# Performance work log

Measured on AMD Instinct MI355X. Metric: run time of the kernel, lower is better.

## Reference

```python
import jax, jax.numpy as jnp
import numpy as np

D_MODEL = 1024
NHEAD = 16
DK = D_MODEL // NHEAD
B, LQ, LK = 4, 2048, 2048


def setup_inputs() -> dict:
    key = jax.random.key(0)
    ks = jax.random.split(key, 11)
    s = 1.0 / np.sqrt(D_MODEL)
    inp = {
        "q": jax.random.normal(ks[0], (B, LQ, D_MODEL), jnp.float32),
        "k": jax.random.normal(ks[1], (B, LK, D_MODEL), jnp.float32),
        "v": jax.random.normal(ks[2], (B, LK, D_MODEL), jnp.float32),
        "attn_mask": jnp.triu(jnp.ones((LQ, LK), dtype=bool), k=1),  # True = masked (causal)
        "Wq": jax.random.normal(ks[3], (D_MODEL, D_MODEL), jnp.float32) * s,
        "bq": jnp.zeros((D_MODEL,), jnp.float32),
        "Wk": jax.random.normal(ks[4], (D_MODEL, D_MODEL), jnp.float32) * s,
        "bk": jnp.zeros((D_MODEL,), jnp.float32),
        "Wv": jax.random.normal(ks[5], (D_MODEL, D_MODEL), jnp.float32) * s,
        "bv": jnp.zeros((D_MODEL,), jnp.float32),
        "Wo": jax.random.normal(ks[6], (D_MODEL, D_MODEL), jnp.float32) * s,
        "bo": jnp.zeros((D_MODEL,), jnp.float32),
    }
    return inp


def _split_heads(x, L):
    # (B, L, D) -> (B, H, L, dk)
    return x.reshape(B, L, NHEAD, DK).transpose(0, 2, 1, 3)


def reference(q, k, v, attn_mask, Wq, bq, Wk, bk, Wv, bv, Wo, bo):
    qh = _split_heads(q @ Wq + bq, LQ)
    kh = _split_heads(k @ Wk + bk, LK)
    vh = _split_heads(v @ Wv + bv, LK)
    scale = 1.0 / np.sqrt(DK).astype(np.float32)
    scores = jnp.einsum("bhqd,bhkd->bhqk", qh, kh) * scale
    scores = jnp.where(attn_mask[None, None, :, :], -jnp.inf, scores)
    attn = jax.nn.softmax(scores, axis=-1)
    ctx = jnp.einsum("bhqk,bhkd->bhqd", attn, vh)
    ctx = ctx.transpose(0, 2, 1, 3).reshape(B, LQ, D_MODEL)
    return ctx @ Wo + bo
```

## Files before the change

### kernel.cpp

```cpp
#include <hip/hip_runtime.h>

#define D_MODEL 1024
#define NHEAD 16
#define DKH 64
#define BATCH 4
#define SEQ 2048
#define MROWS (BATCH*SEQ)

typedef unsigned short u16;
typedef __attribute__((ext_vector_type(8))) short bf16x8;
typedef __attribute__((ext_vector_type(4))) float f32x4;

__device__ __forceinline__ u16 f2bf(float f) {
  union { float f; unsigned int u; } x; x.f = f;
  unsigned int r = x.u + 0x7FFFu + ((x.u >> 16) & 1u);
  return (u16)(r >> 16);
}
__device__ __forceinline__ u16 f2bf_fast(float f) {
  union { float f; unsigned int u; } x; x.f = f;
  return (u16)((x.u + 0x7FFFu) >> 16);
}

__device__ __forceinline__ f32x4 mfma16(bf16x8 a, bf16x8 b, f32x4 c) {
  return __builtin_amdgcn_mfma_f32_16x16x32_bf16(a, b, c, 0, 0, 0);
}

__device__ __forceinline__ void gld_lds16(const void* g, void* l) {
  __builtin_amdgcn_global_load_lds((const __attribute__((address_space(1))) unsigned int*)g,
                                   (__attribute__((address_space(3))) unsigned int*)l, 16, 0, 0);
}

__global__ __launch_bounds__(256) void prep_kernel(
    const float* __restrict__ q, const float* __restrict__ k, const float* __restrict__ v,
    const float* __restrict__ W0, const float* __restrict__ W1,
    const float* __restrict__ W2, const float* __restrict__ W3,
    u16* __restrict__ oq, u16* __restrict__ ok, u16* __restrict__ ov,
    u16* __restrict__ T0, u16* __restrict__ T1,
    u16* __restrict__ T2, u16* __restrict__ T3) {
  const int blk = blockIdx.x;
  const int tid = threadIdx.x;
  if (blk < 24576) {
    const int seg = blk >> 13;
    const int bi = blk & 8191;
    const float* in = (seg == 0) ? q : (seg == 1) ? k : v;
    u16* out = (seg == 0) ? oq : (seg == 1) ? ok : ov;
    int i = (bi * 256 + tid) * 4;
    float4 vv = *(const float4*)(in + i);
    ushort4 o;
    o.x = f2bf(vv.x); o.y = f2bf(vv.y); o.z = f2bf(vv.z); o.w = f2bf(vv.w);
    *(ushort4*)(out + i) = o;
  } else {
    __shared__ float tile[32][33];
    const int t = blk - 24576;
    const int z = t >> 10;
    const int rem = t & 1023;
    const float* W = (z == 0) ? W0 : (z == 1) ? W1 : (z == 2) ? W2 : W3;
    u16* Wt = (z == 0) ? T0 : (z == 1) ? T1 : (z == 2) ? T2 : T3;
    const int bx = (rem & 31) * 32, by = (rem >> 5) * 32;
    const int tx = tid & 31, ty = tid >> 5;
#pragma unroll
    for (int j = 0; j < 32; j += 8)
      tile[ty + j][tx] = W[(size_t)(by + ty + j) * D_MODEL + bx + tx];
    __syncthreads();
#pragma unroll
    for (int j = 0; j < 32; j += 8)
      Wt[(size_t)(bx + ty + j) * D_MODEL + by + tx] = f2bf(tile[tx][ty + j]);
  }
}

template <typename Epi>
__device__ __forceinline__ void gemm_pipe(const u16* __restrict__ Ap,
                                          const u16* __restrict__ Bp,
                                          int m0, int n0g, Epi epi) {
  __shared__ u16 As[2][128 * 64];
  __shared__ u16 Bs[2][128 * 64];
  const int tid = threadIdx.x;
  const int lane = tid & 63;
  const int w = tid >> 6;
  const int wm = w >> 1, wn = w & 1;
  const int lo = lane & 15, g = lane >> 4;
  const int swz = (lo & 7) << 4;
  const int sg = (tid & 7) ^ ((tid >> 3) & 7);
  const int srow = tid >> 3;

  f32x4 acc[4][4] = {};

  auto STAGE_A = [&](int buf, int tt, int j) {
    int row = j * 32 + srow;
    gld_lds16(Ap + (size_t)(m0 + row) * D_MODEL + tt * 64 + sg * 8,
              &As[buf][j * 2048 + tid * 8]);
  };
  auto STAGE_B = [&](int buf, int tt, int j) {
    int row = j * 32 + srow;
    gld_lds16(Bp + (size_t)(n0g + row) * D_MODEL + tt * 64 + sg * 8,
              &Bs[buf][j * 2048 + tid * 8]);
  };

  STAGE_A(0, 0, 0); STAGE_A(0, 0, 1); STAGE_A(0, 0, 2); STAGE_A(0, 0, 3);
  STAGE_B(0, 0, 0); STAGE_B(0, 0, 1); STAGE_B(0, 0, 2); STAGE_B(0, 0, 3);
  STAGE_B(1, 1, 0); STAGE_B(1, 1, 1); STAGE_B(1, 1, 2); STAGE_B(1, 1, 3);
  asm volatile("s_waitcnt vmcnt(4)" ::: "memory");
  __builtin_amdgcn_s_barrier();

  int cur = 0;
#pragma unroll 1
  for (int t = 0; t < 16; ++t) {
    const int nb = cur ^ 1;
    const char* ab = (const char*)&As[cur][0];
    const char* bb2 = (const char*)&Bs[cur][0];

    bf16x8 bf[4][2], af[2][2];
#pragma unroll
    for (int n = 0; n < 4; ++n) {
      int row = wn * 64 + n * 16 + lo;
      bf[n][0] = *(const bf16x8*)(bb2 + row * 128 + ((g * 16) ^ swz));
      bf[n][1] = *(const bf16x8*)(bb2 + row * 128 + ((64 + g * 16) ^ swz));
    }
#pragma unroll
    for (int m = 0; m < 2; ++m) {
      int row = wm * 64 + m * 16 + lo;
      af[m][0] = *(const bf16x8*)(ab + row * 128 + ((g * 16) ^ swz));
      af[m][1] = *(const bf16x8*)(ab + row * 128 + ((64 + g * 16) ^ swz));
    }
    if (t + 1 < 16) {
      STAGE_A(nb, t + 1, 0); STAGE_A(nb, t + 1, 1);
      STAGE_A(nb, t + 1, 2); STAGE_A(nb, t + 1, 3);
    }
    __builtin_amdgcn_s_barrier();
    __builtin_amdgcn_s_setprio(1);
#pragma unroll
    for (int s2 = 0; s2 < 2; ++s2)
#pragma unroll
      for (int m = 0; m < 2; ++m)
#pragma unroll
        for (int n = 0; n < 4; ++n)
          acc[m][n] = mfma16(af[m][s2], bf[n][s2], acc[m][n]);
    __builtin_amdgcn_s_setprio(0);
    __builtin_amdgcn_s_barrier();

    bf16x8 af2[2][2];
#pragma unroll
    for (int m = 0; m < 2; ++m) {
      int row = wm * 64 + (m + 2) * 16 + lo;
      af2[m][0] = *(const bf16x8*)(ab + row * 128 + ((g * 16) ^ swz));
      af2[m][1] = *(const bf16x8*)(ab + row * 128 + ((64 + g * 16) ^ swz));
    }
    if (t + 2 < 16) {
      STAGE_B(cur, t + 2, 0); STAGE_B(cur, t + 2, 1);
      STAGE_B(cur, t + 2, 2); STAGE_B(cur, t + 2, 3);
    }
    __builtin_amdgcn_s_barrier();
    __builtin_amdgcn_s_setprio(1);
#pragma unroll
    for (int s2 = 0; s2 < 2; ++s2)
#pragma unroll
      for (int m = 0; m < 2; ++m)
#pragma unroll
        for (int n = 0; n < 4; ++n)
          acc[m + 2][n] = mfma16(af2[m][s2], bf[n][s2], acc[m + 2][n]);
    __builtin_amdgcn_s_setprio(0);
    if (t + 2 < 16) asm volatile("s_waitcnt vmcnt(4)" ::: "memory");
    else            asm volatile("s_waitcnt vmcnt(0)" ::: "memory");
    __builtin_amdgcn_s_barrier();
    cur = nb;
  }

  epi(acc, wm, wn, lo, g);
}

__global__ __launch_bounds__(256, 2) void gemm_qkv_kernel(
    const u16* __restrict__ Aq, const u16* __restrict__ Ak, const u16* __restrict__ Av,
    const u16* __restrict__ Wt,
    const float* __restrict__ bq, const float* __restrict__ bk, const float* __restrict__ bv,
    u16* __restrict__ Qhd, u16* __restrict__ Khd, u16* __restrict__ Vhd, float qscale) {
  const int flat = blockIdx.x;
  const int swzb = (flat & 7) * 192 + (flat >> 3);
  const int m0 = (swzb / 24) * 128;
  const int n0g = (swzb % 24) * 128;
  const int chunk = n0g >> 10;
  const u16* Ap = (chunk == 0) ? Aq : (chunk == 1) ? Ak : Av;
  const float* bias = (chunk == 0) ? bq : (chunk == 1) ? bk : bv;
  const float scale = (chunk == 0) ? qscale : 1.0f;

  gemm_pipe(Ap, Wt, m0, n0g,
    [&](f32x4 (&acc)[4][4], int wm, int wn, int lo, int g) {
#pragma unroll
      for (int m = 0; m < 4; ++m)
#pragma unroll
        for (int n = 0; n < 4; ++n) {
          int row0 = m0 + wm * 64 + m * 16 + g * 4;
          int colc = (n0g & 1023) + wn * 64 + n * 16 + lo;
          int hh = colc >> 6, d = colc & 63;
          int bb = row0 >> 11;
          float v0 = (acc[m][n][0] + bias[colc]) * scale;
          float v1 = (acc[m][n][1] + bias[colc]) * scale;
          float v2 = (acc[m][n][2] + bias[colc]) * scale;
          float v3 = (acc[m][n][3] + bias[colc]) * scale;
          if (chunk < 2) {
            u16* out = chunk ? Khd : Qhd;
#pragma unroll
            for (int i = 0; i < 4; ++i) {
              int l = (row0 + i) & 2047;
              float vi = (i == 0) ? v0 : (i == 1) ? v1 : (i == 2) ? v2 : v3;
              out[(((size_t)(bb * NHEAD + hh)) * SEQ + l) * DKH + d] = f2bf(vi);
            }
          } else {
            int l = row0 & 2047;
            int kh = (l >> 2) & 7;
            int pos = (l & ~31) | ((2 * (kh & 3) + (kh >> 2)) << 2);
            ushort4 o;
            o.x = f2bf(v0); o.y = f2bf(v1); o.z = f2bf(v2); o.w = f2bf(v3);
            *(ushort4*)&Vhd[(((size_t)(bb * NHEAD + hh)) * DKH + d) * SEQ + pos] = o;
          }
        }
    });
}

__global__ __launch_bounds__(256, 2) void gemm_o_kernel(
    const u16* __restrict__ A, const u16* __restrict__ Bt,
    const float* __restrict__ bias, float* __restrict__ Cout) {
  const int flat = blockIdx.x;
  const int swzb = (flat & 7) * 64 + (flat >> 3);
  const int m0 = (swzb >> 3) * 128;
  const int n0g = (swzb & 7) * 128;

  gemm_pipe(A, Bt, m0, n0g,
    [&](f32x4 (&acc)[4][4], int wm, int wn, int lo, int g) {
#pragma unroll
      for (int m = 0; m < 4; ++m)
#pragma unroll
        for (int n = 0; n < 4; ++n) {
          int row0 = m0 + wm * 64 + m * 16 + g * 4;
          int col = n0g + wn * 64 + n * 16 + lo;
          float bcol = bias[col];
#pragma unroll
          for (int i = 0; i < 4; ++i)
            Cout[(size_t)(row0 + i) * D_MODEL + col] = acc[m][n][i] + bcol;
        }
    });
}

__global__ __launch_bounds__(256, 3) void attn_kernel(
    const u16* __restrict__ Qh, const u16* __restrict__ Kh,
    const u16* __restrict__ Vt, u16* __restrict__ ctx) {
  const int blk = blockIdx.x;
  const int xcd = blk & 7;
  const int local = blk >> 3;
  const int qb = 15 - (local >> 3);
  const int head = xcd * 8 + (local & 7);
  const int b = head >> 4, h = head & (NHEAD - 1);

  const int tid = threadIdx.x;
  const int lane = tid & 63;
  const int w = tid >> 6;
  const int lo = lane & 15, g = lane >> 4;
  const int swz = (lo & 7) << 4;

  __shared__ u16 Ks[3][64 * 64];
  __shared__ u16 Vs[3][64 * 64];

  const size_t hoff = ((size_t)(b * NHEAD + h)) * SEQ * DKH;
  const u16* Qp = Qh + hoff;
  const u16* Kp = Kh + hoff;
  const u16* Vp = Vt + hoff;

  const int nt = 2 * qb + 2;
  const int qmin = qb * 128 + w * 32;

  bf16x8 aq[2][2];
#pragma unroll
  for (int qs = 0; qs < 2; ++qs)
#pragma unroll
    for (int cc = 0; cc < 2; ++cc)
      aq[qs][cc] = *(const bf16x8*)(Qp + (size_t)(qmin + qs * 16 + lo) * DKH + cc * 32 + g * 8);

  const int r_lo = lane >> 3;
  const int sgr = (lane & 7) ^ r_lo;

  auto STAGE = [&](int buf, int t64) {
#pragma unroll
    for (int j = 0; j < 2; ++j) {
      int row = w * 16 + j * 8 + r_lo;
      gld_lds16(Kp + (size_t)(t64 * 64 + row) * DKH + sgr * 8, &Ks[buf][(w * 2 + j) * 512]);
      gld_lds16(Vp + (size_t)row * SEQ + t64 * 64 + sgr * 8, &Vs[buf][(w * 2 + j) * 512]);
    }
  };

  STAGE(0, 0);
  STAGE(1, 1);
  asm volatile("s_waitcnt vmcnt(0)" ::: "memory");
  __builtin_amdgcn_s_barrier();

  f32x4 c[2][4] = {};
  float m_run[2] = {-1e30f, -1e30f}, l_run[2] = {0.f, 0.f};
  int cur = 0;

  for (int kt = 0; kt < nt; ++kt) {
    int b2 = cur + 2; if (b2 >= 3) b2 -= 3;
    if (kt + 2 < nt) STAGE(b2, kt + 2);

    f32x4 s[2][4] = {};
#pragma unroll
    for (int kn = 0; kn < 4; ++kn) {
      const char* krow = (const char*)&Ks[cur][(kn * 16 + lo) * 64];
#pragma unroll
      for (int cc = 0; cc < 2; ++cc) {
        bf16x8 ak = *(const bf16x8*)(krow + ((cc * 64 + g * 16) ^ swz));
        s[0][kn] = mfma16(ak, aq[0][cc], s[0][kn]);
        s[1][kn] = mfma16(ak, aq[1][cc], s[1][kn]);
      }
    }

    if (kt >= nt - 2) {
#pragma unroll
      for (int qs = 0; qs < 2; ++qs) {
        int q = qmin + qs * 16 + lo;
#pragma unroll
        for (int kn = 0; kn < 4; ++kn)
#pragma unroll
          for (int i = 0; i < 4; ++i) {
            int key = kt * 64 + kn * 16 + g * 4 + i;
            if (key > q) s[qs][kn][i] = -1e30f;
          }
      }
    }

    bf16x8 pb[2][2];
#pragma unroll
    for (int qs = 0; qs < 2; ++qs) {
      float mx = s[qs][0][0];
#pragma unroll
      for (int kn = 0; kn < 4; ++kn)
#pragma unroll
        for (int i = 0; i < 4; ++i) mx = fmaxf(mx, s[qs][kn][i]);
      mx = fmaxf(mx, __shfl_xor(mx, 16));
      mx = fmaxf(mx, __shfl_xor(mx, 32));
      if (!__all(mx - m_run[qs] <= 8.0f)) {
        float mnew = fmaxf(m_run[qs], mx);
        float al = __builtin_amdgcn_exp2f(m_run[qs] - mnew);
        m_run[qs] = mnew;
        l_run[qs] *= al;
#pragma unroll
        for (int dn = 0; dn < 4; ++dn) {
          c[qs][dn][0] *= al; c[qs][dn][1] *= al;
          c[qs][dn][2] *= al; c[qs][dn][3] *= al;
        }
      }
      const float mq = m_run[qs];
      float rs = 0.f;
#pragma unroll
      for (int kn = 0; kn < 4; ++kn)
#pragma unroll
        for (int i = 0; i < 4; ++i) {
          float p = __builtin_amdgcn_exp2f(s[qs][kn][i] - mq);
          s[qs][kn][i] = p;
          rs += p;
        }
      rs += __shfl_xor(rs, 16);
      rs += __shfl_xor(rs, 32);
      l_run[qs] += rs;
#pragma unroll
      for (int kc = 0; kc < 2; ++kc) {
        bf16x8 t;
        t[0] = (short)f2bf_fast(s[qs][2 * kc][0]);
        t[1] = (short)f2bf_fast(s[qs][2 * kc][1]);
        t[2] = (short)f2bf_fast(s[qs][2 * kc][2]);
        t[3] = (short)f2bf_fast(s[qs][2 * kc][3]);
        t[4] = (short)f2bf_fast(s[qs][2 * kc + 1][0]);
        t[5] = (short)f2bf_fast(s[qs][2 * kc + 1][1]);
        t[6] = (short)f2bf_fast(s[qs][2 * kc + 1][2]);
        t[7] = (short)f2bf_fast(s[qs][2 * kc + 1][3]);
        pb[qs][kc] = t;
      }
    }

#pragma unroll
    for (int kc = 0; kc < 2; ++kc)
#pragma unroll
      for (int dn = 0; dn < 4; ++dn) {
        const char* vrow = (const char*)&Vs[cur][(dn * 16 + lo) * 64];
        bf16x8 av = *(const bf16x8*)(vrow + ((kc * 64 + g * 16) ^ swz));
        c[0][dn] = mfma16(av, pb[0][kc], c[0][dn]);
        c[1][dn] = mfma16(av, pb[1][kc], c[1][dn]);
      }

    if (kt + 1 < nt) {
      if (kt + 2 < nt) asm volatile("s_waitcnt vmcnt(4)" ::: "memory");
      else             asm volatile("s_waitcnt vmcnt(0)" ::: "memory");
      __builtin_amdgcn_s_barrier();
    }
    cur = (cur == 2) ? 0 : cur + 1;
  }

#pragma unroll
  for (int qs = 0; qs < 2; ++qs) {
    const float rl = 1.0f / l_run[qs];
    const int q = qmin + qs * 16 + lo;
#pragma unroll
    for (int dn = 0; dn < 4; ++dn) {
      ushort4 o;
      o.x = f2bf(c[qs][dn][0] * rl);
      o.y = f2bf(c[qs][dn][1] * rl);
      o.z = f2bf(c[qs][dn][2] * rl);
      o.w = f2bf(c[qs][dn][3] * rl);
      *(ushort4*)&ctx[((size_t)(b * SEQ + q)) * D_MODEL + h * DKH + dn * 16 + g * 4] = o;
    }
  }
}

extern "C" void kernel_launch(void* const* d_in, const int* in_sizes, int n_in,
                              void* d_out, int out_size, void* d_ws, size_t ws_size,
                              hipStream_t stream) {
  const float* q  = (const float*)d_in[0];
  const float* k  = (const float*)d_in[1];
  const float* v  = (const float*)d_in[2];
  const float* Wq = (const float*)d_in[4];
  const float* bq = (const float*)d_in[5];
  const float* Wk = (const float*)d_in[6];
  const float* bk = (const float*)d_in[7];
  const float* Wv = (const float*)d_in[8];
  const float* bv = (const float*)d_in[9];
  const float* Wo = (const float*)d_in[10];
  const float* bo = (const float*)d_in[11];

  char* ws = (char*)d_ws;
  const size_t MB = 1u << 20;
  u16* qb16 = (u16*)(ws + 0 * MB);
  u16* kb16 = (u16*)(ws + 16 * MB);
  u16* vb16 = (u16*)(ws + 32 * MB);
  u16* Wqkvt = (u16*)(ws + 48 * MB);
  u16* Wot  = (u16*)(ws + 54 * MB);
  u16* Qhd  = (u16*)(ws + 56 * MB);
  u16* Khd  = (u16*)(ws + 72 * MB);
  u16* Vhd  = (u16*)(ws + 88 * MB);
  u16* ctxb = qb16;

  u16* Wqt = Wqkvt;
  u16* Wkt = Wqkvt + 1024 * 1024;
  u16* Wvt = Wqkvt + 2 * 1024 * 1024;

  prep_kernel<<<28672, 256, 0, stream>>>(q, k, v, Wq, Wk, Wv, Wo,
                                         qb16, kb16, vb16, Wqt, Wkt, Wvt, Wot);

  const float qscale = 0.125f * 1.4426950408889634f;
  gemm_qkv_kernel<<<1536, 256, 0, stream>>>(qb16, kb16, vb16, Wqkvt,
                                            bq, bk, bv, Qhd, Khd, Vhd, qscale);

  attn_kernel<<<1024, 256, 0, stream>>>(Qhd, Khd, Vhd, ctxb);

  gemm_o_kernel<<<512, 256, 0, stream>>>(ctxb, Wot, bo, (float*)d_out);
}
```

Baseline: 170.9 us.

## Use 256x128 tiles with K=32 steps in QKV projection GEMM

The QKV projection GEMM gets a new pipeline with 256-row by 128-column output tiles. Each of the four waves owns 64 rows across all 128 columns, and the K loop runs in 32-wide steps instead of 64, so the grid halves to 768 blocks. The aim is more reuse of each staged B tile and fewer total global loads, with LDS usage kept about the same. In exchange each thread holds twice the accumulators (128 floats), which may pressure registers at two blocks per CU, and there are fewer blocks to fill the GPU.

New measurement: 177.3 us. +3.8%, slower.

```diff
diff --git a/kernel.cpp b/kernel.cpp
--- a/kernel.cpp
+++ b/kernel.cpp
@@ -69,103 +69,88 @@
 }
 
 template <typename Epi>
-__device__ __forceinline__ void gemm_pipe(const u16* __restrict__ Ap,
-                                          const u16* __restrict__ Bp,
-                                          int m0, int n0g, Epi epi) {
+__device__ __forceinline__ void gemm_pipe2(const u16* __restrict__ Ap,
+                                           const u16* __restrict__ Bp,
+                                           int m0, int n0g, Epi epi) {
   __shared__ u16 As[2][128 * 64];
-  __shared__ u16 Bs[2][128 * 64];
+  __shared__ u16 Bs[2][64 * 64];
   const int tid = threadIdx.x;
   const int lane = tid & 63;
   const int w = tid >> 6;
-  const int wm = w >> 1, wn = w & 1;
   const int lo = lane & 15, g = lane >> 4;
-  const int swz = (lo & 7) << 4;
   const int sg = (tid & 7) ^ ((tid >> 3) & 7);
-  const int srow = tid >> 3;
-
-  f32x4 acc[4][4] = {};
-
-  auto STAGE_A = [&](int buf, int tt, int j) {
-    int row = j * 32 + srow;
-    gld_lds16(Ap + (size_t)(m0 + row) * D_MODEL + tt * 64 + sg * 8,
-              &As[buf][j * 2048 + tid * 8]);
+  const int srow2 = 2 * (tid >> 3) + (sg >> 2);
+  const int scol = (sg & 3) * 8;
+
+  f32x4 acc[4][8] = {};
+
+  auto STAGE_A = [&](int buf, int tt) {
+#pragma unroll
+    for (int j = 0; j < 4; ++j)
+      gld_lds16(Ap + (size_t)(m0 + j * 64 + srow2) * D_MODEL + tt * 32 + scol,
+                &As[buf][j * 2048 + tid * 8]);
   };
-  auto STAGE_B = [&](int buf, int tt, int j) {
-    int row = j * 32 + srow;
-    gld_lds16(Bp + (size_t)(n0g + row) * D_MODEL + tt * 64 + sg * 8,
-              &Bs[buf][j * 2048 + tid * 8]);
+  auto STAGE_B = [&](int buf, int tt) {
+#pragma unroll
+    for (int j = 0; j < 2; ++j)
+      gld_lds16(Bp + (size_t)(n0g + j * 64 + srow2) * D_MODEL + tt * 32 + scol,
+                &Bs[buf][j * 2048 + tid * 8]);
   };
-
-  STAGE_A(0, 0, 0); STAGE_A(0, 0, 1); STAGE_A(0, 0, 2); STAGE_A(0, 0, 3);
-  STAGE_B(0, 0, 0); STAGE_B(0, 0, 1); STAGE_B(0, 0, 2); STAGE_B(0, 0, 3);
-  STAGE_B(1, 1, 0); STAGE_B(1, 1, 1); STAGE_B(1, 1, 2); STAGE_B(1, 1, 3);
-  asm volatile("s_waitcnt vmcnt(4)" ::: "memory");
+  auto RD = [&](const char* base, int R) {
+    int lr = R >> 1;
+    int inner = (((R & 1) << 6) | (g << 4)) ^ ((lr & 7) << 4);
+    return *(const bf16x8*)(base + lr * 128 + inner);
+  };
+
+  STAGE_A(0, 0);
+  STAGE_B(0, 0);
+  STAGE_B(1, 1);
+  asm volatile("s_waitcnt vmcnt(2)" ::: "memory");
   __builtin_amdgcn_s_barrier();
 
-  int cur = 0;
 #pragma unroll 1
-  for (int t = 0; t < 16; ++t) {
+  for (int t = 0; t < 32; ++t) {
+    const int cur = t & 1;
     const int nb = cur ^ 1;
     const char* ab = (const char*)&As[cur][0];
-    const char* bb2 = (const char*)&Bs[cur][0];
-
-    bf16x8 bf[4][2], af[2][2];
-#pragma unroll
-    for (int n = 0; n < 4; ++n) {
-      int row = wn * 64 + n * 16 + lo;
-      bf[n][0] = *(const bf16x8*)(bb2 + row * 128 + ((g * 16) ^ swz));
-      bf[n][1] = *(const bf16x8*)(bb2 + row * 128 + ((64 + g * 16) ^ swz));
-    }
-#pragma unroll
-    for (int m = 0; m < 2; ++m) {
-      int row = wm * 64 + m * 16 + lo;
-      af[m][0] = *(const bf16x8*)(ab + row * 128 + ((g * 16) ^ swz));
-      af[m][1] = *(const bf16x8*)(ab + row * 128 + ((64 + g * 16) ^ swz));
-    }
-    if (t + 1 < 16) {
-      STAGE_A(nb, t + 1, 0); STAGE_A(nb, t + 1, 1);
-      STAGE_A(nb, t + 1, 2); STAGE_A(nb, t + 1, 3);
-    }
+    const char* bb = (const char*)&Bs[cur][0];
+
+    bf16x8 bf[8], af[2];
+#pragma unroll
+    for (int n = 0; n < 8; ++n) bf[n] = RD(bb, n * 16 + lo);
+#pragma unroll
+    for (int m = 0; m < 2; ++m) af[m] = RD(ab, w * 64 + m * 16 + lo);
+    if (t + 1 < 32) STAGE_A(nb, t + 1);
     __builtin_amdgcn_s_barrier();
     __builtin_amdgcn_s_setprio(1);
 #pragma unroll
-    for (int s2 = 0; s2 < 2; ++s2)
-#pragma unroll
-      for (int m = 0; m < 2; ++m)
-#pragma unroll
-        for (int n = 0; n < 4; ++n)
-          acc[m][n] = mfma16(af[m][s2], bf[n][s2], acc[m][n]);
+    for (int m = 0; m < 2; ++m)
+#pragma unroll
+      for (int n = 0; n < 8; ++n)
+        acc[m][n] = mfma16(af[m], bf[n], acc[m][n]);
     __builtin_amdgcn_s_setprio(0);
     __builtin_amdgcn_s_barrier();
 
-    bf16x8 af2[2][2];
-#pragma unroll
-    for (int m = 0; m < 2; ++m) {
-      int row = wm * 64 + (m + 2) * 16 + lo;
-      af2[m][0] = *(const bf16x8*)(ab + row * 128 + ((g * 16) ^ swz));
-      af2[m][1] = *(const bf16x8*)(ab + row * 128 + ((64 + g * 16) ^ swz));
-    }
-    if (t + 2 < 16) {
-      STAGE_B(cur, t + 2, 0); STAGE_B(cur, t + 2, 1);
-      STAGE_B(cur, t + 2, 2); STAGE_B(cur, t + 2, 3);
-    }
+    bf16x8 af2[2];
+#pragma unroll
+    for (int m = 0; m < 2; ++m) af2[m] = RD(ab, w * 64 + (m + 2) * 16 + lo);
+    if (t + 2 < 32) STAGE_B(cur, t + 2);
     __builtin_amdgcn_s_barrier();
     __builtin_amdgcn_s_setprio(1);
 #pragma unroll
-    for (int s2 = 0; s2 < 2; ++s2)
-#pragma unroll
-      for (int m = 0; m < 2; ++m)
-#pragma unroll
-        for (int n = 0; n < 4; ++n)
-          acc[m + 2][n] = mfma16(af2[m][s2], bf[n][s2], acc[m + 2][n]);
+    for (int m = 0; m < 2; ++m)
+#pragma unroll
+      for (int n = 0; n < 8; ++n)
+        acc[m + 2][n] = mfma16(af2[m], bf[n], acc[m + 2][n]);
     __builtin_amdgcn_s_setprio(0);
-    if (t + 2 < 16) asm volatile("s_waitcnt vmcnt(4)" ::: "memory");
-    else            asm volatile("s_waitcnt vmcnt(0)" ::: "memory");
-    __builtin_amdgcn_s_barrier();
-    cur = nb;
+    if (t + 1 < 32) {
+      if (t + 2 < 32) asm volatile("s_waitcnt vmcnt(2)" ::: "memory");
+      else            asm volatile("s_waitcnt vmcnt(0)" ::: "memory");
+      __builtin_amdgcn_s_barrier();
+    }
   }
 
-  epi(acc, wm, wn, lo, g);
+  epi(acc, w, lo, g);
 }
 
 __global__ __launch_bounds__(256, 2) void gemm_qkv_kernel(
@@ -174,22 +159,22 @@
     const float* __restrict__ bq, const float* __restrict__ bk, const float* __restrict__ bv,
     u16* __restrict__ Qhd, u16* __restrict__ Khd, u16* __restrict__ Vhd, float qscale) {
   const int flat = blockIdx.x;
-  const int swzb = (flat & 7) * 192 + (flat >> 3);
-  const int m0 = (swzb / 24) * 128;
+  const int swzb = (flat & 7) * 96 + (flat >> 3);
+  const int m0 = (swzb / 24) * 256;
   const int n0g = (swzb % 24) * 128;
   const int chunk = n0g >> 10;
   const u16* Ap = (chunk == 0) ? Aq : (chunk == 1) ? Ak : Av;
   const float* bias = (chunk == 0) ? bq : (chunk == 1) ? bk : bv;
   const float scale = (chunk == 0) ? qscale : 1.0f;
 
-  gemm_pipe(Ap, Wt, m0, n0g,
-    [&](f32x4 (&acc)[4][4], int wm, int wn, int lo, int g) {
+  gemm_pipe2(Ap, Wt, m0, n0g,
+    [&](f32x4 (&acc)[4][8], int w, int lo, int g) {
 #pragma unroll
       for (int m = 0; m < 4; ++m)
 #pragma unroll
-        for (int n = 0; n < 4; ++n) {
-          int row0 = m0 + wm * 64 + m * 16 + g * 4;
-          int colc = (n0g & 1023) + wn * 64 + n * 16 + lo;
+        for (int n = 0; n < 8; ++n) {
+          int row0 = m0 + w * 64 + m * 16 + g * 4;
+          int colc = (n0g & 1023) + n * 16 + lo;
           int hh = colc >> 6, d = colc & 63;
           int bb = row0 >> 11;
           float v0 = (acc[m][n][0] + bias[colc]) * scale;
@@ -216,6 +201,106 @@
     });
 }
 
+template <typename Epi>
+__device__ __forceinline__ void gemm_pipe(const u16* __restrict__ Ap,
+                                          const u16* __restrict__ Bp,
+                                          int m0, int n0g, Epi epi) {
+  __shared__ u16 As[2][128 * 64];
+  __shared__ u16 Bs[2][128 * 64];
+  const int tid = threadIdx.x;
+  const int lane = tid & 63;
+  const int w = tid >> 6;
+  const int wm = w >> 1, wn = w & 1;
+  const int lo = lane & 15, g = lane >> 4;
+  const int swz = (lo & 7) << 4;
+  const int sg = (tid & 7) ^ ((tid >> 3) & 7);
+  const int srow = tid >> 3;
+
+  f32x4 acc[4][4] = {};
+
+  auto STAGE_A = [&](int buf, int tt, int j) {
+    int row = j * 32 + srow;
+    gld_lds16(Ap + (size_t)(m0 + row) * D_MODEL + tt * 64 + sg * 8,
+              &As[buf][j * 2048 + tid * 8]);
+  };
+  auto STAGE_B = [&](int buf, int tt, int j) {
+    int row = j * 32 + srow;
+    gld_lds16(Bp + (size_t)(n0g + row) * D_MODEL + tt * 64 + sg * 8,
+              &Bs[buf][j * 2048 + tid * 8]);
+  };
+
+  STAGE_A(0, 0, 0); STAGE_A(0, 0, 1); STAGE_A(0, 0, 2); STAGE_A(0, 0, 3);
+  STAGE_B(0, 0, 0); STAGE_B(0, 0, 1); STAGE_B(0, 0, 2); STAGE_B(0, 0, 3);
+  STAGE_B(1, 1, 0); STAGE_B(1, 1, 1); STAGE_B(1, 1, 2); STAGE_B(1, 1, 3);
+  asm volatile("s_waitcnt vmcnt(4)" ::: "memory");
+  __builtin_amdgcn_s_barrier();
+
+  int cur = 0;
+#pragma unroll 1
+  for (int t = 0; t < 16; ++t) {
+    const int nb = cur ^ 1;
+    const char* ab = (const char*)&As[cur][0];
+    const char* bb2 = (const char*)&Bs[cur][0];
+
+    bf16x8 bf[4][2], af[2][2];
+#pragma unroll
+    for (int n = 0; n < 4; ++n) {
+      int row = wn * 64 + n * 16 + lo;
+      bf[n][0] = *(const bf16x8*)(bb2 + row * 128 + ((g * 16) ^ swz));
+      bf[n][1] = *(const bf16x8*)(bb2 + row * 128 + ((64 + g * 16) ^ swz));
+    }
+#pragma unroll
+    for (int m = 0; m < 2; ++m) {
+      int row = wm * 64 + m * 16 + lo;
+      af[m][0] = *(const bf16x8*)(ab + row * 128 + ((g * 16) ^ swz));
+      af[m][1] = *(const bf16x8*)(ab + row * 128 + ((64 + g * 16) ^ swz));
+    }
+    if (t + 1 < 16) {
+      STAGE_A(nb, t + 1, 0); STAGE_A(nb, t + 1, 1);
+      STAGE_A(nb, t + 1, 2); STAGE_A(nb, t + 1, 3);
+    }
+    __builtin_amdgcn_s_barrier();
+    __builtin_amdgcn_s_setprio(1);
+#pragma unroll
+    for (int s2 = 0; s2 < 2; ++s2)
+#pragma unroll
+      for (int m = 0; m < 2; ++m)
+#pragma unroll
+        for (int n = 0; n < 4; ++n)
+          acc[m][n] = mfma16(af[m][s2], bf[n][s2], acc[m][n]);
+    __builtin_amdgcn_s_setprio(0);
+    __builtin_amdgcn_s_barrier();
+
+    bf16x8 af2[2][2];
+#pragma unroll
+    for (int m = 0; m < 2; ++m) {
+      int row = wm * 64 + (m + 2) * 16 + lo;
+      af2[m][0] = *(const bf16x8*)(ab + row * 128 + ((g * 16) ^ swz));
+      af2[m][1] = *(const bf16x8*)(ab + row * 128 + ((64 + g * 16) ^ swz));
+    }
+    if (t + 2 < 16) {
+      STAGE_B(cur, t + 2, 0); STAGE_B(cur, t + 2, 1);
+      STAGE_B(cur, t + 2, 2); STAGE_B(cur, t + 2, 3);
+    }
+    __builtin_amdgcn_s_barrier();
+    __builtin_amdgcn_s_setprio(1);
+#pragma unroll
+    for (int s2 = 0; s2 < 2; ++s2)
+#pragma unroll
+      for (int m = 0; m < 2; ++m)
+#pragma unroll
+        for (int n = 0; n < 4; ++n)
+          acc[m + 2][n] = mfma16(af2[m][s2], bf[n][s2], acc[m + 2][n]);
+    __builtin_amdgcn_s_setprio(0);
+    if (t + 2 < 16) asm volatile("s_waitcnt vmcnt(4)" ::: "memory");
+    else            asm volatile("s_waitcnt vmcnt(0)" ::: "memory");
+    __builtin_amdgcn_s_barrier();
+    cur = nb;
+  }
+
+  epi(acc, wm, wn, lo, g);
+}
+
 __global__ __launch_bounds__(256, 2) void gemm_o_kernel(
     const u16* __restrict__ A, const u16* __restrict__ Bt,
     const float* __restrict__ bias, float* __restrict__ Cout) {
@@ -443,8 +528,8 @@
                                          qb16, kb16, vb16, Wqt, Wkt, Wvt, Wot);
 
   const float qscale = 0.125f * 1.4426950408889634f;
-  gemm_qkv_kernel<<<1536, 256, 0, stream>>>(qb16, kb16, vb16, Wqkvt,
-                                            bq, bk, bv, Qhd, Khd, Vhd, qscale);
+  gemm_qkv_kernel<<<768, 256, 0, stream>>>(qb16, kb16, vb16, Wqkvt,
+                                           bq, bk, bv, Qhd, Khd, Vhd, qscale);
 
   attn_kernel<<<1024, 256, 0, stream>>>(Qhd, Khd, Vhd, ctxb);
 
```
